# Optimization experiments

Measured on AMD Instinct MI355X. Metric: run time of the kernel, lower is better.

## Reference

```python
import jax, jax.numpy as jnp
import numpy as np
from jax import lax

B, CIN, COUT, K = 4, 128, 128, 3
Z = X = Y = 32
EPS = 1e-8


def setup_inputs() -> dict:
    key = jax.random.key(0)
    k1, k2, k3 = jax.random.split(key, 3)
    x = jax.random.normal(k1, (B, CIN, Z, X, Y), dtype=jnp.float32)
    S = jax.random.normal(k2, (B, CIN), dtype=jnp.float32)
    weight = jax.random.normal(k3, (COUT, CIN, K, K, K), dtype=jnp.float32)
    return {"x": x, "S": S, "weight": weight}


def reference(x, S, weight):
    b, cin, z, xx, yy = x.shape
    cout = weight.shape[0]
    # Per-sample modulated weight: [B, cout, cin, k, k, k]
    W = weight[None] * (S[:, None, :, None, None, None] + 1.0)
    # Demodulation: L2-normalize each (b, cout) filter
    d = lax.rsqrt(jnp.sum(W * W, axis=(2, 3, 4, 5), keepdims=True) + EPS)
    W = W * d
    # Grouped conv3d with groups=B (stride=1, dilation=1 -> same padding = (k-1)//2)
    pad = (K - 1) // 2
    xr = x.reshape(1, b * cin, z, xx, yy)
    Wr = W.reshape(b * cout, cin, K, K, K)
    out = lax.conv_general_dilated(
        xr, Wr,
        window_strides=(1, 1, 1),
        padding=[(pad, pad)] * 3,
        feature_group_count=b,
        dimension_numbers=("NCDHW", "OIDHW", "NCDHW"),
    )
    return out.reshape(b, cout, z, xx, yy)
```

## Files before the change

### kernel.cpp

```cpp
#include <hip/hip_runtime.h>

#define B_    4
#define CIN_  128
#define COUT_ 128
#define EPSF  1e-8f

typedef short  short8  __attribute__((ext_vector_type(8)));
typedef unsigned short ushort8 __attribute__((ext_vector_type(8)));
typedef float  f32x16  __attribute__((ext_vector_type(16)));

#define GLOAD_LDS16(g, l) __builtin_amdgcn_global_load_lds( \
    (const __attribute__((address_space(1))) unsigned int*)(g), \
    (__attribute__((address_space(3))) unsigned int*)(l), 16, 0, 0)

__device__ __forceinline__ unsigned short f2bf(float f) {
    union { float f; unsigned int u; } v; v.f = f;
    unsigned int r = (v.u + 0x7fffu + ((v.u >> 16) & 1u)) >> 16;
    return (unsigned short)r;
}

__global__ __launch_bounds__(128) void scale_kernel(const float* __restrict__ S,
                                                    const float* __restrict__ w,
                                                    float* __restrict__ d) {
    const int co = blockIdx.x;
    const int ci = threadIdx.x;
    const float* wp = w + ((size_t)co * CIN_ + ci) * 27;
    float wsq = 0.f;
#pragma unroll
    for (int k = 0; k < 27; ++k) { float v = wp[k]; wsq += v * v; }
    __shared__ float red[128];
    for (int b = 0; b < B_; ++b) {
        float s = S[b * CIN_ + ci] + 1.0f;
        red[ci] = s * s * wsq;
        __syncthreads();
        for (int off = 64; off > 0; off >>= 1) {
            if (ci < off) red[ci] += red[ci + off];
            __syncthreads();
        }
        if (ci == 0) d[b * COUT_ + co] = rsqrtf(red[0] + EPSF);
        __syncthreads();
    }
}

__global__ __launch_bounds__(256) void wt_kernel(const float* __restrict__ w,
                                                 unsigned short* __restrict__ wtf) {
    int idx = blockIdx.x * 256 + threadIdx.x;
    int e  = idx & 7;
    int l  = (idx >> 3) & 63;
    int c  = (idx >> 9) & 7;
    int ct = (idx >> 12) & 3;
    int ko = idx >> 14;
    int co = ct * 32 + (l & 31);
    int ci = c * 16 + (l >> 5) * 8 + e;
    wtf[idx] = f2bf(w[((size_t)co * CIN_ + ci) * 27 + ko]);
}

__global__ __launch_bounds__(256) void xt_kernel(const float* __restrict__ x,
                                                 const float* __restrict__ S,
                                                 unsigned short* __restrict__ xT) {
    __shared__ float ls[128 * 33];
    const int xx = blockIdx.x, z = blockIdx.y, b = blockIdx.z;
    const int tid = threadIdx.x;
    const size_t base = (size_t)b * 4194304 + (size_t)z * 1024 + xx * 32;
#pragma unroll
    for (int it = 0; it < 4; ++it) {
        int i = tid + it * 256;
        int ci = i >> 3, y4 = (i & 7) * 4;
        float4 v = *(const float4*)(x + base + (size_t)ci * 32768 + y4);
        float s = S[b * CIN_ + ci] + 1.0f;
        ls[ci * 33 + y4 + 0] = v.x * s;
        ls[ci * 33 + y4 + 1] = v.y * s;
        ls[ci * 33 + y4 + 2] = v.z * s;
        ls[ci * 33 + y4 + 3] = v.w * s;
    }
    __syncthreads();
    const size_t obase = (size_t)((b * 32 + z) * 32 + xx) * 4096;
#pragma unroll
    for (int it = 0; it < 2; ++it) {
        int i = tid + it * 256;
        int y = i >> 4, c = (i >> 1) & 7, h = i & 1;
        ushort8 v;
#pragma unroll
        for (int j = 0; j < 8; ++j) v[j] = f2bf(ls[(c * 16 + h * 8 + j) * 33 + y]);
        *(ushort8*)(xT + obase + c * 512 + y * 16 + h * 8) = v;
    }
}

__global__ __launch_bounds__(256, 3) void conv_mfma(const unsigned short* __restrict__ xT,
                                                    const unsigned short* __restrict__ wtf,
                                                    const float* __restrict__ dscale,
                                                    const char* __restrict__ zpage,
                                                    float* __restrict__ out) {
    __shared__ char smem[2][17408];
    const int tid  = threadIdx.x;
    const int lane = tid & 63;
    const int cog  = tid >> 6;
    const int z0 = (blockIdx.x >> 4) * 2;
    const int x0 = (blockIdx.x & 15) * 2;
    const int b  = blockIdx.y;

    const char* xTb = (const char*)xT;
    const char* gsrc[5];
#pragma unroll
    for (int s = 0; s < 5; ++s) {
        int g = (s < 4) ? (tid + s * 256) : (1024 + tid);
        int row = g / 68, rem = g - row * 68;
        int h = rem / 34, yi = rem - h * 34;
        int zg = z0 + (row >> 2) - 1;
        int xg = x0 + (row & 3) - 1;
        bool ok = (g < 1088) && ((unsigned)zg < 32u) && ((unsigned)xg < 32u) &&
                  (yi >= 1) && (yi <= 32);
        gsrc[s] = ok ? (xTb + ((((b * 32 + zg) * 32 + xg) * 8192) + (yi - 1) * 32 + h * 16))
                     : zpage;
    }

    const int bperlane = ((lane >> 5) * 34 + (lane & 31)) * 16;
    const int aperlane = lane * 16;
    const char* wtb = (const char*)wtf;

    f32x16 acc[2][2];
#pragma unroll
    for (int cz = 0; cz < 2; ++cz)
#pragma unroll
        for (int cx = 0; cx < 2; ++cx)
#pragma unroll
            for (int r = 0; r < 16; ++r) acc[cz][cx][r] = 0.f;

#pragma unroll
    for (int s = 0; s < 4; ++s)
        GLOAD_LDS16(gsrc[s], &smem[0][tid * 16 + s * 4096]);
    if (tid < 64)
        GLOAD_LDS16(gsrc[4], &smem[0][16384 + tid * 16]);
    __syncthreads();

    for (int c = 0; c < 8; ++c) {
        if (c < 7) {
            const int nb = (c + 1) & 1;
            const int coff = (c + 1) * 1024;
#pragma unroll
            for (int s = 0; s < 4; ++s)
                GLOAD_LDS16(gsrc[s] + coff, &smem[nb][tid * 16 + s * 4096]);
            if (tid < 64)
                GLOAD_LDS16(gsrc[4] + coff, &smem[nb][16384 + tid * 16]);
        }
        const char* buf   = smem[c & 1];
        const char* abase = wtb + c * 1024 + cog * 8192;
#pragma unroll
        for (int ky = 0; ky < 3; ++ky) {
            short8 a[9];
#pragma unroll
            for (int t = 0; t < 9; ++t)
                a[t] = *(const short8*)(abase + (t * 3 + ky) * 32768 + aperlane);
            short8 bf[2][4];
#pragma unroll
            for (int xr = 0; xr < 4; ++xr)
                bf[0][xr] = *(const short8*)(buf + (xr * 68 + ky) * 16 + bperlane);
#pragma unroll
            for (int zr = 0; zr < 4; ++zr) {
                if (zr < 3) {
#pragma unroll
                    for (int xr = 0; xr < 4; ++xr)
                        bf[(zr + 1) & 1][xr] = *(const short8*)(buf +
                            (((zr + 1) * 4 + xr) * 68 + ky) * 16 + bperlane);
                }
                __builtin_amdgcn_s_setprio(1);
#pragma unroll
                for (int cz = 0; cz < 2; ++cz) {
                    const int kz = zr - cz;
                    if (kz >= 0 && kz <= 2) {
                        const short8* bb = bf[zr & 1];
                        acc[cz][0] = __builtin_amdgcn_mfma_f32_32x32x16_bf16(a[kz*3+0], bb[0], acc[cz][0], 0, 0, 0);
                        acc[cz][1] = __builtin_amdgcn_mfma_f32_32x32x16_bf16(a[kz*3+0], bb[1], acc[cz][1], 0, 0, 0);
                        acc[cz][0] = __builtin_amdgcn_mfma_f32_32x32x16_bf16(a[kz*3+1], bb[1], acc[cz][0], 0, 0, 0);
                        acc[cz][1] = __builtin_amdgcn_mfma_f32_32x32x16_bf16(a[kz*3+1], bb[2], acc[cz][1], 0, 0, 0);
                        acc[cz][0] = __builtin_amdgcn_mfma_f32_32x32x16_bf16(a[kz*3+2], bb[2], acc[cz][0], 0, 0, 0);
                        acc[cz][1] = __builtin_amdgcn_mfma_f32_32x32x16_bf16(a[kz*3+2], bb[3], acc[cz][1], 0, 0, 0);
                    }
                }
                __builtin_amdgcn_s_setprio(0);
            }
        }
        __syncthreads();
    }

    float dd[16];
#pragma unroll
    for (int r = 0; r < 16; ++r)
        dd[r] = dscale[b * COUT_ + cog * 32 + (r & 3) + 8 * (r >> 2) + 4 * (lane >> 5)];
#pragma unroll
    for (int cz = 0; cz < 2; ++cz)
#pragma unroll
    for (int cx = 0; cx < 2; ++cx) {
        size_t ob = (((size_t)(b * COUT_ + cog * 32) * 32 + (z0 + cz)) * 32 + (x0 + cx)) * 32 + (lane & 31);
#pragma unroll
        for (int r = 0; r < 16; ++r) {
            int row = (r & 3) + 8 * (r >> 2) + 4 * (lane >> 5);
            out[ob + (size_t)row * 32768] = acc[cz][cx][r] * dd[r];
        }
    }
}

__global__ __launch_bounds__(256, 4) void conv_kernel(const float* __restrict__ x,
                                                      const float* __restrict__ S,
                                                      const float* __restrict__ w,
                                                      const float* __restrict__ dscale,
                                                      float* __restrict__ out) {
    __shared__ float xs[6][6][36];
    __shared__ float wsm[27][16];
    const int tid = threadIdx.x;
    const int zt  = blockIdx.x >> 3;
    const int xt  = blockIdx.x & 7;
    const int co0 = blockIdx.y * 16;
    const int b   = blockIdx.z;
    const int z0 = zt * 4, x0 = xt * 4;
    const int lane = tid & 63;
    const int cg = tid >> 6;
    const int zz = (lane >> 4) & 3;
    const int xx = (lane >> 2) & 3;
    const int y0 = (lane & 3) * 8;
    float acc[4][8];
#pragma unroll
    for (int c = 0; c < 4; ++c)
#pragma unroll
        for (int j = 0; j < 8; ++j) acc[c][j] = 0.f;
    for (int ci = 0; ci < CIN_; ++ci) {
        __syncthreads();
        const float* xb = x + (size_t)(b * CIN_ + ci) * 32768;
        const float smod = S[b * CIN_ + ci] + 1.0f;
#pragma unroll
        for (int t = 0; t < 5; ++t) {
            int i = tid + t * 256;
            if (i < 6 * 6 * 34) {
                int zi = i / 204, r = i - zi * 204, xi = r / 34, yi = r - xi * 34;
                int z = z0 + zi - 1, xc = x0 + xi - 1, y = yi - 1;
                float v = 0.f;
                if ((unsigned)z < 32u && (unsigned)xc < 32u && (unsigned)y < 32u)
                    v = xb[z * 1024 + xc * 32 + y] * smod;
                xs[zi][xi][yi] = v;
            }
        }
#pragma unroll
        for (int t = 0; t < 2; ++t) {
            int i = tid + t * 256;
            if (i < 16 * 27) {
                int cog2 = i / 27, k = i - cog2 * 27;
                wsm[k][cog2] = w[((size_t)(co0 + cog2) * CIN_ + ci) * 27 + k];
            }
        }
        __syncthreads();
#pragma unroll
        for (int kz = 0; kz < 3; ++kz)
#pragma unroll
        for (int kx = 0; kx < 3; ++kx) {
            const float* xrow = &xs[zz + kz][xx + kx][y0];
            float xw[10];
#pragma unroll
            for (int q = 0; q < 10; ++q) xw[q] = xrow[q];
            const int kb = (kz * 3 + kx) * 3;
#pragma unroll
            for (int ky = 0; ky < 3; ++ky) {
                float4 wvv = *(const float4*)&wsm[kb + ky][cg * 4];
#pragma unroll
                for (int j = 0; j < 8; ++j) {
                    acc[0][j] = fmaf(xw[ky + j], wvv.x, acc[0][j]);
                    acc[1][j] = fmaf(xw[ky + j], wvv.y, acc[1][j]);
                    acc[2][j] = fmaf(xw[ky + j], wvv.z, acc[2][j]);
                    acc[3][j] = fmaf(xw[ky + j], wvv.w, acc[3][j]);
                }
            }
        }
    }
#pragma unroll
    for (int c = 0; c < 4; ++c) {
        const int co = co0 + cg * 4 + c;
        const float dd = dscale[b * COUT_ + co];
        float* ob = out + (((size_t)(b * COUT_ + co) * 32 + (z0 + zz)) * 32 + (x0 + xx)) * 32 + y0;
#pragma unroll
        for (int j = 0; j < 8; ++j) ob[j] = acc[c][j] * dd;
    }
}

extern "C" void kernel_launch(void* const* d_in, const int* in_sizes, int n_in,
                              void* d_out, int out_size, void* d_ws, size_t ws_size,
                              hipStream_t stream) {
    const float* x = (const float*)d_in[0];
    const float* S = (const float*)d_in[1];
    const float* w = (const float*)d_in[2];
    float* out = (float*)d_out;

    const size_t NEED = 1048576 + 33554432;
    if (ws_size >= NEED) {
        float* dscale = (float*)d_ws;
        char*  zpage  = (char*)d_ws + 4096;
        unsigned short* wtf = (unsigned short*)((char*)d_ws + 12288);
        unsigned short* xT  = (unsigned short*)((char*)d_ws + 1048576);
        hipMemsetAsync(zpage, 0, 8192, stream);
        scale_kernel<<<dim3(COUT_), dim3(128), 0, stream>>>(S, w, dscale);
        wt_kernel<<<dim3(1728), dim3(256), 0, stream>>>(w, wtf);
        xt_kernel<<<dim3(32, 32, 4), dim3(256), 0, stream>>>(x, S, xT);
        conv_mfma<<<dim3(256, 4), dim3(256), 0, stream>>>(xT, wtf, dscale, zpage, out);
    } else {
        float* dscale = (float*)d_ws;
        scale_kernel<<<dim3(COUT_), dim3(128), 0, stream>>>(S, w, dscale);
        conv_kernel<<<dim3(64, 8, 4), dim3(256), 0, stream>>>(x, S, w, dscale, out);
    }
}
```

Baseline: 134.5 us.

## Enlarge conv tile to 4x4 spatial with 8 waves and phased staged loads

The MFMA conv block grows from a 2x2 (z,x) output tile with 4 waves to a 4x4 tile with 8 waves of 512 threads. Each wave now computes 4 z-rows by 2 x-columns, which improves halo reuse of the input slab (6x6 rows loaded instead of 4x4 per 2x2 output). The per-chunk loop is split into six phases by ky and z-group. Next-chunk global-to-LDS loads are interleaved between phases, weight fragments are prefetched ahead, and extra s_barriers are added. Costs include doubled LDS, only 256 blocks at one block per CU, and higher register pressure from 8 accumulators plus three A-fragment sets.

```diff
diff --git a/kernel.cpp b/kernel.cpp
--- a/kernel.cpp
+++ b/kernel.cpp
@@ -86,29 +86,68 @@
     }
 }
 
-__global__ __launch_bounds__(256, 3) void conv_mfma(const unsigned short* __restrict__ xT,
+template<int KY, int G>
+__device__ __forceinline__ void phase_mfma(const char* buf, int xh2, int bperlane,
+                                           const short8* a, f32x16 (&acc)[4][2]) {
+    short8 bf[2][4];
+#pragma unroll
+    for (int xr = 0; xr < 4; ++xr)
+        bf[0][xr] = *(const short8*)(buf + (((G * 3) * 6 + xh2 + xr) * 68 + KY) * 16 + bperlane);
+    __builtin_amdgcn_s_barrier();
+#pragma unroll
+    for (int j = 0; j < 3; ++j) {
+        const int zr = G * 3 + j;
+        if (j < 2) {
+#pragma unroll
+            for (int xr = 0; xr < 4; ++xr)
+                bf[(j + 1) & 1][xr] = *(const short8*)(buf +
+                    (((zr + 1) * 6 + xh2 + xr) * 68 + KY) * 16 + bperlane);
+        }
+        __builtin_amdgcn_s_setprio(1);
+#pragma unroll
+        for (int cz = 0; cz < 4; ++cz) {
+            const int kz = zr - cz;
+            if (kz >= 0 && kz <= 2) {
+                const short8* bb = bf[j & 1];
+                acc[cz][0] = __builtin_amdgcn_mfma_f32_32x32x16_bf16(a[kz*3+0], bb[0], acc[cz][0], 0,0,0);
+                acc[cz][1] = __builtin_amdgcn_mfma_f32_32x32x16_bf16(a[kz*3+0], bb[1], acc[cz][1], 0,0,0);
+                acc[cz][0] = __builtin_amdgcn_mfma_f32_32x32x16_bf16(a[kz*3+1], bb[1], acc[cz][0], 0,0,0);
+                acc[cz][1] = __builtin_amdgcn_mfma_f32_32x32x16_bf16(a[kz*3+1], bb[2], acc[cz][1], 0,0,0);
+                acc[cz][0] = __builtin_amdgcn_mfma_f32_32x32x16_bf16(a[kz*3+2], bb[2], acc[cz][0], 0,0,0);
+                acc[cz][1] = __builtin_amdgcn_mfma_f32_32x32x16_bf16(a[kz*3+2], bb[3], acc[cz][1], 0,0,0);
+            }
+        }
+        __builtin_amdgcn_s_setprio(0);
+    }
+    __builtin_amdgcn_s_barrier();
+}
+
+__global__ __launch_bounds__(512, 1) void conv_mfma(const unsigned short* __restrict__ xT,
                                                     const unsigned short* __restrict__ wtf,
                                                     const float* __restrict__ dscale,
                                                     const char* __restrict__ zpage,
                                                     float* __restrict__ out) {
-    __shared__ char smem[2][17408];
+    __shared__ char smem[2][39168];
     const int tid  = threadIdx.x;
     const int lane = tid & 63;
-    const int cog  = tid >> 6;
-    const int z0 = (blockIdx.x >> 4) * 2;
-    const int x0 = (blockIdx.x & 15) * 2;
+    const int wv   = tid >> 6;
+    const int cog  = wv & 3;
+    const int xh2  = (wv >> 2) * 2;
+    const int z0 = (blockIdx.x >> 3) * 4;
+    const int x0 = (blockIdx.x & 7) * 4;
     const int b  = blockIdx.y;
 
     const char* xTb = (const char*)xT;
     const char* gsrc[5];
 #pragma unroll
     for (int s = 0; s < 5; ++s) {
-        int g = (s < 4) ? (tid + s * 256) : (1024 + tid);
+        int g = tid + s * 512;
         int row = g / 68, rem = g - row * 68;
         int h = rem / 34, yi = rem - h * 34;
-        int zg = z0 + (row >> 2) - 1;
-        int xg = x0 + (row & 3) - 1;
-        bool ok = (g < 1088) && ((unsigned)zg < 32u) && ((unsigned)xg < 32u) &&
+        int zi = row / 6, xi = row - zi * 6;
+        int zg = z0 + zi - 1;
+        int xg = x0 + xi - 1;
+        bool ok = (g < 2448) && ((unsigned)zg < 32u) && ((unsigned)xg < 32u) &&
                   (yi >= 1) && (yi <= 32);
         gsrc[s] = ok ? (xTb + ((((b * 32 + zg) * 32 + xg) * 8192) + (yi - 1) * 32 + h * 16))
                      : zpage;
@@ -118,9 +157,9 @@
     const int aperlane = lane * 16;
     const char* wtb = (const char*)wtf;
 
-    f32x16 acc[2][2];
-#pragma unroll
-    for (int cz = 0; cz < 2; ++cz)
+    f32x16 acc[4][2];
+#pragma unroll
+    for (int cz = 0; cz < 4; ++cz)
 #pragma unroll
         for (int cx = 0; cx < 2; ++cx)
 #pragma unroll
@@ -128,70 +167,59 @@
 
 #pragma unroll
     for (int s = 0; s < 4; ++s)
-        GLOAD_LDS16(gsrc[s], &smem[0][tid * 16 + s * 4096]);
-    if (tid < 64)
-        GLOAD_LDS16(gsrc[4], &smem[0][16384 + tid * 16]);
+        GLOAD_LDS16(gsrc[s], &smem[0][tid * 16 + s * 8192]);
+    if (tid < 400)
+        GLOAD_LDS16(gsrc[4], &smem[0][tid * 16 + 32768]);
     __syncthreads();
 
+#define STAGE(s)                                                                 \
+    if (c < 7) {                                                                 \
+        if ((s) < 4) { GLOAD_LDS16(gsrc[(s)] + coff, nbuf + tid * 16 + (s) * 8192); } \
+        else if (tid < 400) { GLOAD_LDS16(gsrc[4] + coff, nbuf + tid * 16 + 32768); } \
+    }
+
     for (int c = 0; c < 8; ++c) {
-        if (c < 7) {
-            const int nb = (c + 1) & 1;
-            const int coff = (c + 1) * 1024;
-#pragma unroll
-            for (int s = 0; s < 4; ++s)
-                GLOAD_LDS16(gsrc[s] + coff, &smem[nb][tid * 16 + s * 4096]);
-            if (tid < 64)
-                GLOAD_LDS16(gsrc[4] + coff, &smem[nb][16384 + tid * 16]);
-        }
         const char* buf   = smem[c & 1];
+        char*       nbuf  = (char*)smem[(c + 1) & 1];
+        const int   coff  = (c + 1) * 1024;
         const char* abase = wtb + c * 1024 + cog * 8192;
-#pragma unroll
-        for (int ky = 0; ky < 3; ++ky) {
-            short8 a[9];
-#pragma unroll
-            for (int t = 0; t < 9; ++t)
-                a[t] = *(const short8*)(abase + (t * 3 + ky) * 32768 + aperlane);
-            short8 bf[2][4];
-#pragma unroll
-            for (int xr = 0; xr < 4; ++xr)
-                bf[0][xr] = *(const short8*)(buf + (xr * 68 + ky) * 16 + bperlane);
-#pragma unroll
-            for (int zr = 0; zr < 4; ++zr) {
-                if (zr < 3) {
-#pragma unroll
-                    for (int xr = 0; xr < 4; ++xr)
-                        bf[(zr + 1) & 1][xr] = *(const short8*)(buf +
-                            (((zr + 1) * 4 + xr) * 68 + ky) * 16 + bperlane);
-                }
-                __builtin_amdgcn_s_setprio(1);
-#pragma unroll
-                for (int cz = 0; cz < 2; ++cz) {
-                    const int kz = zr - cz;
-                    if (kz >= 0 && kz <= 2) {
-                        const short8* bb = bf[zr & 1];
-                        acc[cz][0] = __builtin_amdgcn_mfma_f32_32x32x16_bf16(a[kz*3+0], bb[0], acc[cz][0], 0, 0, 0);
-                        acc[cz][1] = __builtin_amdgcn_mfma_f32_32x32x16_bf16(a[kz*3+0], bb[1], acc[cz][1], 0, 0, 0);
-                        acc[cz][0] = __builtin_amdgcn_mfma_f32_32x32x16_bf16(a[kz*3+1], bb[1], acc[cz][0], 0, 0, 0);
-                        acc[cz][1] = __builtin_amdgcn_mfma_f32_32x32x16_bf16(a[kz*3+1], bb[2], acc[cz][1], 0, 0, 0);
-                        acc[cz][0] = __builtin_amdgcn_mfma_f32_32x32x16_bf16(a[kz*3+2], bb[2], acc[cz][0], 0, 0, 0);
-                        acc[cz][1] = __builtin_amdgcn_mfma_f32_32x32x16_bf16(a[kz*3+2], bb[3], acc[cz][1], 0, 0, 0);
-                    }
-                }
-                __builtin_amdgcn_s_setprio(0);
-            }
-        }
-        __syncthreads();
-    }
+
+        short8 a0[9], a1[9], a2[9];
+#pragma unroll
+        for (int t = 0; t < 9; ++t)
+            a0[t] = *(const short8*)(abase + (t * 3 + 0) * 32768 + aperlane);
+
+        STAGE(0);
+        phase_mfma<0, 0>(buf, xh2, bperlane, a0, acc);
+#pragma unroll
+        for (int t = 0; t < 9; ++t)
+            a1[t] = *(const short8*)(abase + (t * 3 + 1) * 32768 + aperlane);
+        STAGE(1);
+        phase_mfma<0, 1>(buf, xh2, bperlane, a0, acc);
+        STAGE(2);
+        phase_mfma<1, 0>(buf, xh2, bperlane, a1, acc);
+#pragma unroll
+        for (int t = 0; t < 9; ++t)
+            a2[t] = *(const short8*)(abase + (t * 3 + 2) * 32768 + aperlane);
+        STAGE(3);
+        phase_mfma<1, 1>(buf, xh2, bperlane, a1, acc);
+        STAGE(4);
+        phase_mfma<2, 0>(buf, xh2, bperlane, a2, acc);
+        phase_mfma<2, 1>(buf, xh2, bperlane, a2, acc);
+
+        __syncthreads();
+    }
+#undef STAGE
 
     float dd[16];
 #pragma unroll
     for (int r = 0; r < 16; ++r)
         dd[r] = dscale[b * COUT_ + cog * 32 + (r & 3) + 8 * (r >> 2) + 4 * (lane >> 5)];
 #pragma unroll
-    for (int cz = 0; cz < 2; ++cz)
+    for (int cz = 0; cz < 4; ++cz)
 #pragma unroll
     for (int cx = 0; cx < 2; ++cx) {
-        size_t ob = (((size_t)(b * COUT_ + cog * 32) * 32 + (z0 + cz)) * 32 + (x0 + cx)) * 32 + (lane & 31);
+        size_t ob = (((size_t)(b * COUT_ + cog * 32) * 32 + (z0 + cz)) * 32 + (x0 + xh2 + cx)) * 32 + (lane & 31);
 #pragma unroll
         for (int r = 0; r < 16; ++r) {
             int row = (r & 3) + 8 * (r >> 2) + 4 * (lane >> 5);
@@ -298,7 +326,7 @@
         scale_kernel<<<dim3(COUT_), dim3(128), 0, stream>>>(S, w, dscale);
         wt_kernel<<<dim3(1728), dim3(256), 0, stream>>>(w, wtf);
         xt_kernel<<<dim3(32, 32, 4), dim3(256), 0, stream>>>(x, S, xT);
-        conv_mfma<<<dim3(256, 4), dim3(256), 0, stream>>>(xT, wtf, dscale, zpage, out);
+        conv_mfma<<<dim3(64, 4), dim3(512), 0, stream>>>(xT, wtf, dscale, zpage, out);
     } else {
         float* dscale = (float*)d_ws;
         scale_kernel<<<dim3(COUT_), dim3(128), 0, stream>>>(S, w, dscale);
```

Result: faster. 123.1 us (-8.4%).
